# Kernel optimization log

Hardware: AMD Instinct MI355X
Metric: run time of the kernel (lower is better)

The kernel has to match this reference:

```python
import jax, jax.numpy as jnp
import numpy as np

N = 50000
E = 500000
D = 512


def setup_inputs() -> dict:
    key = jax.random.key(0)
    ks = jax.random.split(key, 16)
    inp = {
        'h': jax.random.normal(ks[0], (N, D), jnp.float32),
        's': jax.random.normal(ks[1], (N, D), jnp.float32),
        'm': jax.random.normal(ks[2], (N, D), jnp.float32),
        'norm_g': jax.random.uniform(ks[3], (N, 1), jnp.float32),
        'norm_f': jax.random.uniform(ks[4], (N, 1), jnp.float32),
        'src_g': jax.random.randint(ks[5], (E,), 0, N, jnp.int32),
        'dst_g': jax.random.randint(ks[6], (E,), 0, N, jnp.int32),
        'src_f': jax.random.randint(ks[7], (E,), 0, N, jnp.int32),
        'dst_f': jax.random.randint(ks[8], (E,), 0, N, jnp.int32),
        'wh': jax.random.normal(ks[9], (D, D), jnp.float32) / np.sqrt(D),
        'ws': jax.random.normal(ks[10], (D, D), jnp.float32) / np.sqrt(D),
        'wm': jax.random.normal(ks[11], (D, D), jnp.float32) / np.sqrt(D),
        'bh': jax.random.normal(ks[12], (D,), jnp.float32) * 0.02,
        'bs': jax.random.normal(ks[13], (D,), jnp.float32) * 0.02,
        'bm': jax.random.normal(ks[14], (D,), jnp.float32) * 0.02,
    }
    return inp


def reference(h, s, m, norm_g, norm_f, src_g, dst_g, src_f, dst_f, wh, ws, wm, bh, bs, bm):
    n = h.shape[0]
    # dense projections
    h = (h @ wh) * norm_g          # [N,D]
    s = (s @ ws) * norm_f          # [N,D]
    m = m @ wm                     # [N,D] global skip
    # dual GCN aggregation: copy_src + sum over edges, then norm scaling
    h = jax.ops.segment_sum(h[src_g], dst_g, num_segments=n) * norm_g
    s = jax.ops.segment_sum(s[src_f], dst_f, num_segments=n) * norm_f
    # bias add + three-way residual sum + activation
    out = (h + bh) + (s + bs) + (m + bm)
    return jax.nn.relu(out)
```

## Files before the change

kernel.cpp:

```cpp
#include <hip/hip_runtime.h>
#include <hip/hip_bf16.h>
#include <cstdint>
#include <cstddef>

#define DD 512
#define D4 128

typedef unsigned short u16;
typedef unsigned int u32;
typedef short s8v __attribute__((ext_vector_type(8)));
typedef float f4v __attribute__((ext_vector_type(4)));

__device__ __forceinline__ u16 f2bf(float f) {
  u32 u = __builtin_bit_cast(u32, f);
  u = (u + 0x7FFFu + ((u >> 16) & 1u)) >> 16;
  return (u16)u;
}
__device__ __forceinline__ float bf2f(u16 h) {
  u32 u = ((u32)h) << 16;
  return __builtin_bit_cast(float, u);
}

__device__ __forceinline__ void glds16(const void* g, void* l) {
  __builtin_amdgcn_global_load_lds(
      (const __attribute__((address_space(1))) void*)g,
      (__attribute__((address_space(3))) void*)l, 16, 0, 0);
}


__global__ void hist_kernel(const int* __restrict__ dg, const int* __restrict__ df,
                            int* __restrict__ deg_g, int* __restrict__ deg_f, int E) {
  int i = blockIdx.x * blockDim.x + threadIdx.x;
  int total = 2 * E;
  int stride = gridDim.x * blockDim.x;
  for (; i < total; i += stride) {
    if (i < E) atomicAdd(&deg_g[dg[i]], 1);
    else       atomicAdd(&deg_f[df[i - E]], 1);
  }
}

__global__ void scan_kernel(const int* __restrict__ deg_g, const int* __restrict__ deg_f,
                            int* __restrict__ rp_g, int* __restrict__ rp_f,
                            int* __restrict__ cur_g, int* __restrict__ cur_f, int N) {
  const int* deg = (blockIdx.x == 0) ? deg_g : deg_f;
  int* rp  = (blockIdx.x == 0) ? rp_g  : rp_f;
  int* cur = (blockIdx.x == 0) ? cur_g : cur_f;
  __shared__ int sums[256];
  int t = threadIdx.x;
  int strip = (N + 255) / 256;
  int base = t * strip;
  int lim = N - base; if (lim > strip) lim = strip; if (lim < 0) lim = 0;
  int s = 0;
  for (int j = 0; j < lim; ++j) s += deg[base + j];
  sums[t] = s;
  __syncthreads();
  for (int off = 1; off < 256; off <<= 1) {
    int v = sums[t];
    int add = (t >= off) ? sums[t - off] : 0;
    __syncthreads();
    sums[t] = v + add;
    __syncthreads();
  }
  int run = (t == 0) ? 0 : sums[t - 1];
  for (int j = 0; j < lim; ++j) {
    rp[base + j] = run;
    cur[base + j] = run;
    run += deg[base + j];
  }
  if (t == 255) rp[N] = sums[255];
}

__global__ void fill_kernel(const int* __restrict__ src, const int* __restrict__ dst,
                            int* __restrict__ cur, int* __restrict__ csr, int E) {
  int i = blockIdx.x * blockDim.x + threadIdx.x;
  int stride = gridDim.x * blockDim.x;
  for (; i < E; i += stride) {
    int d = dst[i];
    int pos = atomicAdd(&cur[d], 1);
    csr[pos] = src[i];
  }
}


__global__ __launch_bounds__(256) void conv_bf16_kernel(const float* __restrict__ in,
                                                        u16* __restrict__ outb, int total4) {
  int i = blockIdx.x * blockDim.x + threadIdx.x;
  int stride = gridDim.x * blockDim.x;
  for (; i < total4; i += stride) {
    float4 v = ((const float4*)in)[i];
    ushort4 o = make_ushort4(f2bf(v.x), f2bf(v.y), f2bf(v.z), f2bf(v.w));
    ((ushort4*)outb)[i] = o;
  }
}


__global__ __launch_bounds__(128) void gather_kernel(const u16* __restrict__ featb,
    const float* __restrict__ norm, const int* __restrict__ rp, const int* __restrict__ csr,
    u16* __restrict__ XHi, u16* __restrict__ XLo, int N) {
  int i = blockIdx.x;
  if (i >= N) return;
  int c = threadIdx.x;
  const ushort4* f8 = (const ushort4*)featb;
  float a0 = 0.f, a1 = 0.f, a2 = 0.f, a3 = 0.f;
  int b = rp[i], e = rp[i + 1];
  int j = b;
  for (; j + 4 <= e; j += 4) {
    int s0 = csr[j], s1 = csr[j + 1], s2 = csr[j + 2], s3 = csr[j + 3];
    float g0 = norm[s0], g1 = norm[s1], g2 = norm[s2], g3 = norm[s3];
    ushort4 v0 = f8[(size_t)s0 * D4 + c];
    ushort4 v1 = f8[(size_t)s1 * D4 + c];
    ushort4 v2 = f8[(size_t)s2 * D4 + c];
    ushort4 v3 = f8[(size_t)s3 * D4 + c];
    a0 += g0 * bf2f(v0.x) + g1 * bf2f(v1.x) + g2 * bf2f(v2.x) + g3 * bf2f(v3.x);
    a1 += g0 * bf2f(v0.y) + g1 * bf2f(v1.y) + g2 * bf2f(v2.y) + g3 * bf2f(v3.y);
    a2 += g0 * bf2f(v0.z) + g1 * bf2f(v1.z) + g2 * bf2f(v2.z) + g3 * bf2f(v3.z);
    a3 += g0 * bf2f(v0.w) + g1 * bf2f(v1.w) + g2 * bf2f(v2.w) + g3 * bf2f(v3.w);
  }
  for (; j < e; ++j) {
    int s = csr[j];
    float gs = norm[s];
    ushort4 v = f8[(size_t)s * D4 + c];
    a0 += gs * bf2f(v.x); a1 += gs * bf2f(v.y); a2 += gs * bf2f(v.z); a3 += gs * bf2f(v.w);
  }
  float gi = norm[i];
  float o0 = a0 * gi, o1 = a1 * gi, o2 = a2 * gi, o3 = a3 * gi;
  u16 h0 = f2bf(o0), h1 = f2bf(o1), h2 = f2bf(o2), h3 = f2bf(o3);
  ushort4 hv = make_ushort4(h0, h1, h2, h3);
  ushort4 lv = make_ushort4(f2bf(o0 - bf2f(h0)), f2bf(o1 - bf2f(h1)),
                            f2bf(o2 - bf2f(h2)), f2bf(o3 - bf2f(h3)));
  *(ushort4*)(XHi + (size_t)i * DD + c * 4) = hv;
  *(ushort4*)(XLo + (size_t)i * DD + c * 4) = lv;
}


__global__ __launch_bounds__(256) void wsplit_kernel(
    const float* __restrict__ wh, const float* __restrict__ ws, const float* __restrict__ wm,
    u16* __restrict__ WtHi, u16* __restrict__ WtLo) {
  __shared__ float tile[64][65];
  int si = blockIdx.y;
  const float* W = (si == 0) ? wh : (si == 1) ? ws : wm;
  int tb = blockIdx.x;
  int kb = (tb >> 3) << 6;
  int cb = (tb & 7) << 6;
  int t = threadIdx.x;
#pragma unroll
  for (int i = 0; i < 16; ++i) {
    int idx = t + (i << 8);
    int kr = idx >> 6, cc = idx & 63;
    tile[kr][cc] = W[(size_t)(kb + kr) * DD + cb + cc];
  }
  __syncthreads();
  size_t base = (size_t)si * DD * DD;
#pragma unroll
  for (int i = 0; i < 16; ++i) {
    int idx = t + (i << 8);
    int cr = idx >> 6, kk = idx & 63;
    float v = tile[kk][cr];
    u16 hi = f2bf(v);
    u16 lo = f2bf(v - bf2f(hi));
    size_t off = base + (size_t)(cb + cr) * DD + kb + kk;
    WtHi[off] = hi;
    WtLo[off] = lo;
  }
}


#define BM 128
#define BN 256
#define BK 32

__global__ __launch_bounds__(256, 2) void gemm3_mfma(
    const u16* __restrict__ XhHi, const u16* __restrict__ XhLo,
    const u16* __restrict__ XsHi, const u16* __restrict__ XsLo,
    const float* __restrict__ Mm,
    const u16* __restrict__ WtHi, const u16* __restrict__ WtLo,
    const float* __restrict__ bh, const float* __restrict__ bs, const float* __restrict__ bm,
    float* __restrict__ out, int Mrows) {
  __shared__ u16 sAh[BM * BK];
  __shared__ u16 sAl[BM * BK];
  __shared__ u16 sBh[BN * BK];
  __shared__ u16 sBl[BN * BK];

  int tid = threadIdx.x;
  int wv = tid >> 6;
  int lane = tid & 63;
  int bm0 = blockIdx.y * BM;
  int bn0 = blockIdx.x * BN;

  f4v acc[8][4];
#pragma unroll
  for (int i = 0; i < 8; ++i)
#pragma unroll
    for (int j = 0; j < 4; ++j) acc[i][j] = (f4v){0.f, 0.f, 0.f, 0.f};

  for (int si = 0; si < 3; ++si) {
    const u16* AH = (si == 0) ? XhHi : XsHi;
    const u16* AL = (si == 0) ? XhLo : XsLo;
    const u16* WH = WtHi + (size_t)si * DD * DD;
    const u16* WL = WtLo + (size_t)si * DD * DD;
    for (int k0 = 0; k0 < DD; k0 += BK) {
      {
        int colo = lane >> 2;
        int chunk = lane & 3;
#pragma unroll
        for (int i = 0; i < 4; ++i) {
          int cg = wv * 4 + i;
          int lcol = cg * 16 + colo;
          int sw = (lcol >> 1) & 3;
          const u16* gh = WH + (size_t)(bn0 + lcol) * DD + k0 + ((chunk ^ sw) * 8);
          const u16* gl = WL + (size_t)(bn0 + lcol) * DD + k0 + ((chunk ^ sw) * 8);
          glds16(gh, (char*)sBh + cg * 1024);
          glds16(gl, (char*)sBl + cg * 1024);
        }
      }
      if (si < 2) {
        int rowo = lane >> 2;
        int chunk = lane & 3;
#pragma unroll
        for (int i = 0; i < 2; ++i) {
          int rg = wv * 2 + i;
          int lrow = rg * 16 + rowo;
          int sw = (lrow >> 1) & 3;
          int grow = bm0 + lrow;
          if (grow >= Mrows) grow = Mrows - 1;
          const u16* gh = AH + (size_t)grow * DD + k0 + ((chunk ^ sw) * 8);
          const u16* gl = AL + (size_t)grow * DD + k0 + ((chunk ^ sw) * 8);
          glds16(gh, (char*)sAh + rg * 1024);
          glds16(gl, (char*)sAl + rg * 1024);
        }
      } else {
        float4 vv[4];
#pragma unroll
        for (int i = 0; i < 4; ++i) {
          int idx = tid + (i << 8);
          int row = idx >> 3;
          int gr = bm0 + row;
          int kc = idx & 7;
          vv[i] = make_float4(0.f, 0.f, 0.f, 0.f);
          if (gr < Mrows) vv[i] = *(const float4*)(Mm + (size_t)gr * DD + k0 + kc * 4);
        }
#pragma unroll
        for (int i = 0; i < 4; ++i) {
          int idx = tid + (i << 8);
          int row = idx >> 3;
          int kc = idx & 7;
          int sw = (row >> 1) & 3;
          int off = row * 32 + (((kc >> 1) ^ sw) * 8) + (kc & 1) * 4;
          float4 v = vv[i];
          u16 h0 = f2bf(v.x), h1 = f2bf(v.y), h2 = f2bf(v.z), h3 = f2bf(v.w);
          u16 l0 = f2bf(v.x - bf2f(h0)), l1 = f2bf(v.y - bf2f(h1));
          u16 l2 = f2bf(v.z - bf2f(h2)), l3 = f2bf(v.w - bf2f(h3));
          uint2 ph = make_uint2((u32)h0 | ((u32)h1 << 16), (u32)h2 | ((u32)h3 << 16));
          uint2 pl = make_uint2((u32)l0 | ((u32)l1 << 16), (u32)l2 | ((u32)l3 << 16));
          *(uint2*)(sAh + off) = ph;
          *(uint2*)(sAl + off) = pl;
        }
      }
      __syncthreads();
      int c16 = lane >> 4;
      int rr = lane & 15;
      s8v bhf[4], blf[4];
#pragma unroll
      for (int ng = 0; ng < 4; ++ng) {
        int col = wv * 64 + ng * 16 + rr;
        int sw = (col >> 1) & 3;
        bhf[ng] = *(const s8v*)(sBh + col * 32 + ((c16 ^ sw) * 8));
        blf[ng] = *(const s8v*)(sBl + col * 32 + ((c16 ^ sw) * 8));
      }
#pragma unroll
      for (int mg = 0; mg < 8; ++mg) {
        int row = mg * 16 + rr;
        int sw = (row >> 1) & 3;
        s8v ah = *(const s8v*)(sAh + row * 32 + ((c16 ^ sw) * 8));
        s8v al = *(const s8v*)(sAl + row * 32 + ((c16 ^ sw) * 8));
#pragma unroll
        for (int ng = 0; ng < 4; ++ng) {
          acc[mg][ng] = __builtin_amdgcn_mfma_f32_16x16x32_bf16(ah, bhf[ng], acc[mg][ng], 0, 0, 0);
          acc[mg][ng] = __builtin_amdgcn_mfma_f32_16x16x32_bf16(al, bhf[ng], acc[mg][ng], 0, 0, 0);
          acc[mg][ng] = __builtin_amdgcn_mfma_f32_16x16x32_bf16(ah, blf[ng], acc[mg][ng], 0, 0, 0);
        }
      }
      __syncthreads();
    }
  }

  int rr = lane & 15;
  int rgrp = lane >> 4;
  float bias[4];
#pragma unroll
  for (int ng = 0; ng < 4; ++ng) {
    int col = bn0 + wv * 64 + ng * 16 + rr;
    bias[ng] = bh[col] + bs[col] + bm[col];
  }
#pragma unroll
  for (int mg = 0; mg < 8; ++mg) {
#pragma unroll
    for (int r = 0; r < 4; ++r) {
      int row = bm0 + mg * 16 + rgrp * 4 + r;
      if (row < Mrows) {
#pragma unroll
        for (int ng = 0; ng < 4; ++ng) {
          int col = bn0 + wv * 64 + ng * 16 + rr;
          float v = acc[mg][ng][r] + bias[ng];
          out[(size_t)row * DD + col] = v > 0.f ? v : 0.f;
        }
      }
    }
  }
}


extern "C" void kernel_launch(void* const* d_in, const int* in_sizes, int n_in,
                              void* d_out, int out_size, void* d_ws, size_t ws_size,
                              hipStream_t stream) {
  const float* h   = (const float*)d_in[0];
  const float* s   = (const float*)d_in[1];
  const float* m   = (const float*)d_in[2];
  const float* ng  = (const float*)d_in[3];
  const float* nf  = (const float*)d_in[4];
  const int* src_g = (const int*)d_in[5];
  const int* dst_g = (const int*)d_in[6];
  const int* src_f = (const int*)d_in[7];
  const int* dst_f = (const int*)d_in[8];
  const float* wh  = (const float*)d_in[9];
  const float* wsp = (const float*)d_in[10];
  const float* wm  = (const float*)d_in[11];
  const float* bh  = (const float*)d_in[12];
  const float* bs  = (const float*)d_in[13];
  const float* bm  = (const float*)d_in[14];
  float* out = (float*)d_out;

  int N = in_sizes[3];
  int E = in_sizes[5];

  u16* XhHi = (u16*)d_ws;
  u16* XhLo = XhHi + (size_t)N * DD;
  u16* XsHi = XhLo + (size_t)N * DD;
  u16* XsLo = XsHi + (size_t)N * DD;
  u16* featb = XsLo + (size_t)N * DD;
  u16* WtHi = featb + (size_t)N * DD;
  u16* WtLo = WtHi + (size_t)3 * DD * DD;
  int* deg_g = (int*)(WtLo + (size_t)3 * DD * DD);
  int* deg_f = deg_g + N;
  int* rp_g  = deg_f + N;
  int* rp_f  = rp_g + (N + 1);
  int* cur_g = rp_f + (N + 1);
  int* cur_f = cur_g + N;
  int* csr_g = cur_f + N;
  int* csr_f = csr_g + E;

  int total4 = (N * DD) / 4;

  hipMemsetAsync(deg_g, 0, 2 * (size_t)N * sizeof(int), stream);
  wsplit_kernel<<<dim3(64, 3), 256, 0, stream>>>(wh, wsp, wm, WtHi, WtLo);
  hist_kernel<<<2048, 256, 0, stream>>>(dst_g, dst_f, deg_g, deg_f, E);
  scan_kernel<<<2, 256, 0, stream>>>(deg_g, deg_f, rp_g, rp_f, cur_g, cur_f, N);
  fill_kernel<<<2048, 256, 0, stream>>>(src_g, dst_g, cur_g, csr_g, E);
  fill_kernel<<<2048, 256, 0, stream>>>(src_f, dst_f, cur_f, csr_f, E);
  conv_bf16_kernel<<<2048, 256, 0, stream>>>(h, featb, total4);
  gather_kernel<<<N, 128, 0, stream>>>(featb, ng, rp_g, csr_g, XhHi, XhLo, N);
  conv_bf16_kernel<<<2048, 256, 0, stream>>>(s, featb, total4);
  gather_kernel<<<N, 128, 0, stream>>>(featb, nf, rp_f, csr_f, XsHi, XsLo, N);

  dim3 gg(DD / BN, (N + BM - 1) / BM);
  gemm3_mfma<<<gg, 256, 0, stream>>>(XhHi, XhLo, XsHi, XsLo, m, WtHi, WtLo,
                                     bh, bs, bm, out, N);
}
```

Measured before the change: 985.3 us.

## Presplit m to bf16 hi/lo, widen gather to wave-per-node, XCD-aware GEMM tile order

The m matrix is now split into bf16 hi/lo arrays by a separate pass, so the GEMM's third stage loads it through the same async global-to-LDS path as the other operands instead of converting fp32 in registers. The gather kernel now assigns one wavefront per destination node and loads 8 bf16 values per lane. The GEMM grid is flattened and block IDs are remapped so that neighbouring tiles land on the same XCD for L2 reuse. The extra conversion pass adds a full read of m plus writes of two bf16 copies, in exchange for a simpler and more async GEMM inner loop.

```diff
diff --git a/kernel.cpp b/kernel.cpp
--- a/kernel.cpp
+++ b/kernel.cpp
@@ -10,6 +10,7 @@
 typedef unsigned int u32;
 typedef short s8v __attribute__((ext_vector_type(8)));
 typedef float f4v __attribute__((ext_vector_type(4)));
+typedef u16 u16v8 __attribute__((ext_vector_type(8)));
 
 __device__ __forceinline__ u16 f2bf(float f) {
   u32 u = __builtin_bit_cast(u32, f);
@@ -94,42 +95,63 @@
 }
 
 
-__global__ __launch_bounds__(128) void gather_kernel(const u16* __restrict__ featb,
+__global__ __launch_bounds__(256) void convsplit_kernel(const float* __restrict__ in,
+                                                        u16* __restrict__ hi, u16* __restrict__ lo,
+                                                        int total4) {
+  int i = blockIdx.x * blockDim.x + threadIdx.x;
+  int stride = gridDim.x * blockDim.x;
+  for (; i < total4; i += stride) {
+    float4 v = ((const float4*)in)[i];
+    u16 h0 = f2bf(v.x), h1 = f2bf(v.y), h2 = f2bf(v.z), h3 = f2bf(v.w);
+    ((ushort4*)hi)[i] = make_ushort4(h0, h1, h2, h3);
+    ((ushort4*)lo)[i] = make_ushort4(f2bf(v.x - bf2f(h0)), f2bf(v.y - bf2f(h1)),
+                                     f2bf(v.z - bf2f(h2)), f2bf(v.w - bf2f(h3)));
+  }
+}
+
+
+__global__ __launch_bounds__(256) void gather_kernel(const u16* __restrict__ featb,
     const float* __restrict__ norm, const int* __restrict__ rp, const int* __restrict__ csr,
     u16* __restrict__ XHi, u16* __restrict__ XLo, int N) {
-  int i = blockIdx.x;
+  int w = threadIdx.x >> 6;
+  int lane = threadIdx.x & 63;
+  int i = blockIdx.x * 4 + w;
   if (i >= N) return;
-  int c = threadIdx.x;
-  const ushort4* f8 = (const ushort4*)featb;
-  float a0 = 0.f, a1 = 0.f, a2 = 0.f, a3 = 0.f;
+  const u16v8* f8 = (const u16v8*)featb;
+  float a[8];
+#pragma unroll
+  for (int t = 0; t < 8; ++t) a[t] = 0.f;
   int b = rp[i], e = rp[i + 1];
   int j = b;
   for (; j + 4 <= e; j += 4) {
     int s0 = csr[j], s1 = csr[j + 1], s2 = csr[j + 2], s3 = csr[j + 3];
     float g0 = norm[s0], g1 = norm[s1], g2 = norm[s2], g3 = norm[s3];
-    ushort4 v0 = f8[(size_t)s0 * D4 + c];
-    ushort4 v1 = f8[(size_t)s1 * D4 + c];
-    ushort4 v2 = f8[(size_t)s2 * D4 + c];
-    ushort4 v3 = f8[(size_t)s3 * D4 + c];
-    a0 += g0 * bf2f(v0.x) + g1 * bf2f(v1.x) + g2 * bf2f(v2.x) + g3 * bf2f(v3.x);
-    a1 += g0 * bf2f(v0.y) + g1 * bf2f(v1.y) + g2 * bf2f(v2.y) + g3 * bf2f(v3.y);
-    a2 += g0 * bf2f(v0.z) + g1 * bf2f(v1.z) + g2 * bf2f(v2.z) + g3 * bf2f(v3.z);
-    a3 += g0 * bf2f(v0.w) + g1 * bf2f(v1.w) + g2 * bf2f(v2.w) + g3 * bf2f(v3.w);
+    u16v8 v0 = f8[(size_t)s0 * 64 + lane];
+    u16v8 v1 = f8[(size_t)s1 * 64 + lane];
+    u16v8 v2 = f8[(size_t)s2 * 64 + lane];
+    u16v8 v3 = f8[(size_t)s3 * 64 + lane];
+#pragma unroll
+    for (int t = 0; t < 8; ++t)
+      a[t] += g0 * bf2f(v0[t]) + g1 * bf2f(v1[t]) + g2 * bf2f(v2[t]) + g3 * bf2f(v3[t]);
   }
   for (; j < e; ++j) {
     int s = csr[j];
     float gs = norm[s];
-    ushort4 v = f8[(size_t)s * D4 + c];
-    a0 += gs * bf2f(v.x); a1 += gs * bf2f(v.y); a2 += gs * bf2f(v.z); a3 += gs * bf2f(v.w);
+    u16v8 v = f8[(size_t)s * 64 + lane];
+#pragma unroll
+    for (int t = 0; t < 8; ++t) a[t] += gs * bf2f(v[t]);
   }
   float gi = norm[i];
-  float o0 = a0 * gi, o1 = a1 * gi, o2 = a2 * gi, o3 = a3 * gi;
-  u16 h0 = f2bf(o0), h1 = f2bf(o1), h2 = f2bf(o2), h3 = f2bf(o3);
-  ushort4 hv = make_ushort4(h0, h1, h2, h3);
-  ushort4 lv = make_ushort4(f2bf(o0 - bf2f(h0)), f2bf(o1 - bf2f(h1)),
-                            f2bf(o2 - bf2f(h2)), f2bf(o3 - bf2f(h3)));
-  *(ushort4*)(XHi + (size_t)i * DD + c * 4) = hv;
-  *(ushort4*)(XLo + (size_t)i * DD + c * 4) = lv;
+  u16v8 hv, lv;
+#pragma unroll
+  for (int t = 0; t < 8; ++t) {
+    float o = a[t] * gi;
+    u16 hh = f2bf(o);
+    hv[t] = hh;
+    lv[t] = f2bf(o - bf2f(hh));
+  }
+  *(u16v8*)(XHi + (size_t)i * DD + lane * 8) = hv;
+  *(u16v8*)(XLo + (size_t)i * DD + lane * 8) = lv;
 }
 
 
@@ -172,7 +194,7 @@
 __global__ __launch_bounds__(256, 2) void gemm3_mfma(
     const u16* __restrict__ XhHi, const u16* __restrict__ XhLo,
     const u16* __restrict__ XsHi, const u16* __restrict__ XsLo,
-    const float* __restrict__ Mm,
+    const u16* __restrict__ MHi,  const u16* __restrict__ MLo,
     const u16* __restrict__ WtHi, const u16* __restrict__ WtLo,
     const float* __restrict__ bh, const float* __restrict__ bs, const float* __restrict__ bm,
     float* __restrict__ out, int Mrows) {
@@ -184,8 +206,14 @@
   int tid = threadIdx.x;
   int wv = tid >> 6;
   int lane = tid & 63;
-  int bm0 = blockIdx.y * BM;
-  int bn0 = blockIdx.x * BN;
+
+  int nwg = gridDim.x;
+  int orig = blockIdx.x;
+  int q = nwg >> 3, r = nwg & 7;
+  int xcd = orig & 7, pos = orig >> 3;
+  int sid = (xcd < r ? xcd * (q + 1) : r * (q + 1) + (xcd - r) * q) + pos;
+  int bn0 = (sid & 1) * BN;
+  int bm0 = (sid >> 1) * BM;
 
   f4v acc[8][4];
 #pragma unroll
@@ -194,8 +222,8 @@
     for (int j = 0; j < 4; ++j) acc[i][j] = (f4v){0.f, 0.f, 0.f, 0.f};
 
   for (int si = 0; si < 3; ++si) {
-    const u16* AH = (si == 0) ? XhHi : XsHi;
-    const u16* AL = (si == 0) ? XhLo : XsLo;
+    const u16* AH = (si == 0) ? XhHi : (si == 1) ? XsHi : MHi;
+    const u16* AL = (si == 0) ? XhLo : (si == 1) ? XsLo : MLo;
     const u16* WH = WtHi + (size_t)si * DD * DD;
     const u16* WL = WtLo + (size_t)si * DD * DD;
     for (int k0 = 0; k0 < DD; k0 += BK) {
@@ -213,7 +241,7 @@
           glds16(gl, (char*)sBl + cg * 1024);
         }
       }
-      if (si < 2) {
+      {
         int rowo = lane >> 2;
         int chunk = lane & 3;
 #pragma unroll
@@ -227,33 +255,6 @@
           const u16* gl = AL + (size_t)grow * DD + k0 + ((chunk ^ sw) * 8);
           glds16(gh, (char*)sAh + rg * 1024);
           glds16(gl, (char*)sAl + rg * 1024);
-        }
-      } else {
-        float4 vv[4];
-#pragma unroll
-        for (int i = 0; i < 4; ++i) {
-          int idx = tid + (i << 8);
-          int row = idx >> 3;
-          int gr = bm0 + row;
-          int kc = idx & 7;
-          vv[i] = make_float4(0.f, 0.f, 0.f, 0.f);
-          if (gr < Mrows) vv[i] = *(const float4*)(Mm + (size_t)gr * DD + k0 + kc * 4);
-        }
-#pragma unroll
-        for (int i = 0; i < 4; ++i) {
-          int idx = tid + (i << 8);
-          int row = idx >> 3;
-          int kc = idx & 7;
-          int sw = (row >> 1) & 3;
-          int off = row * 32 + (((kc >> 1) ^ sw) * 8) + (kc & 1) * 4;
-          float4 v = vv[i];
-          u16 h0 = f2bf(v.x), h1 = f2bf(v.y), h2 = f2bf(v.z), h3 = f2bf(v.w);
-          u16 l0 = f2bf(v.x - bf2f(h0)), l1 = f2bf(v.y - bf2f(h1));
-          u16 l2 = f2bf(v.z - bf2f(h2)), l3 = f2bf(v.w - bf2f(h3));
-          uint2 ph = make_uint2((u32)h0 | ((u32)h1 << 16), (u32)h2 | ((u32)h3 << 16));
-          uint2 pl = make_uint2((u32)l0 | ((u32)l1 << 16), (u32)l2 | ((u32)l3 << 16));
-          *(uint2*)(sAh + off) = ph;
-          *(uint2*)(sAl + off) = pl;
         }
       }
       __syncthreads();
@@ -337,8 +338,10 @@
   u16* XhLo = XhHi + (size_t)N * DD;
   u16* XsHi = XhLo + (size_t)N * DD;
   u16* XsLo = XsHi + (size_t)N * DD;
-  u16* featb = XsLo + (size_t)N * DD;
-  u16* WtHi = featb + (size_t)N * DD;
+  u16* MHi  = XsLo + (size_t)N * DD;
+  u16* MLo  = MHi + (size_t)N * DD;
+  u16* featb = MHi;
+  u16* WtHi = MLo + (size_t)N * DD;
   u16* WtLo = WtHi + (size_t)3 * DD * DD;
   int* deg_g = (int*)(WtLo + (size_t)3 * DD * DD);
   int* deg_f = deg_g + N;
@@ -358,11 +361,13 @@
   fill_kernel<<<2048, 256, 0, stream>>>(src_g, dst_g, cur_g, csr_g, E);
   fill_kernel<<<2048, 256, 0, stream>>>(src_f, dst_f, cur_f, csr_f, E);
   conv_bf16_kernel<<<2048, 256, 0, stream>>>(h, featb, total4);
-  gather_kernel<<<N, 128, 0, stream>>>(featb, ng, rp_g, csr_g, XhHi, XhLo, N);
+  gather_kernel<<<(N + 3) / 4, 256, 0, stream>>>(featb, ng, rp_g, csr_g, XhHi, XhLo, N);
   conv_bf16_kernel<<<2048, 256, 0, stream>>>(s, featb, total4);
-  gather_kernel<<<N, 128, 0, stream>>>(featb, nf, rp_f, csr_f, XsHi, XsLo, N);
-
-  dim3 gg(DD / BN, (N + BM - 1) / BM);
-  gemm3_mfma<<<gg, 256, 0, stream>>>(XhHi, XhLo, XsHi, XsLo, m, WtHi, WtLo,
-                                     bh, bs, bm, out, N);
-}
+  gather_kernel<<<(N + 3) / 4, 256, 0, stream>>>(featb, nf, rp_f, csr_f, XsHi, XsLo, N);
+  convsplit_kernel<<<2048, 256, 0, stream>>>(m, MHi, MLo, total4);
+
+  int nrb = (N + BM - 1) / BM;
+  int nwg = (DD / BN) * nrb;
+  gemm3_mfma<<<nwg, 256, 0, stream>>>(XhHi, XhLo, XsHi, XsLo, MHi, MLo, WtHi, WtLo,
+                                      bh, bs, bm, out, N);
+}
```

Result: faster. 956.2 us (-2.9%).
